# Kernel tuning notes

Hardware: AMD Instinct MI355X
Metric: run time of the kernel (lower is better)

The kernel has to match this reference:

```python
import jax, jax.numpy as jnp
import numpy as np

N = 50000        # nodes
E = 400000       # edges (no self-loops; self-loops appended in forward)
IN_DIM = 128
H, C = 4, 64     # heads, channels per head
D = H * C        # 256
NEG_SLOPE = 0.2


def setup_inputs() -> dict:
    key = jax.random.key(0)
    ks = jax.random.split(key, 8)
    x = jax.random.normal(ks[0], (N, IN_DIM), jnp.float32)
    # build edges with no self-loops (src != dst), matching the module's mask
    src = jax.random.randint(ks[1], (E,), 0, N)
    off = jax.random.randint(ks[2], (E,), 1, N)
    dst = (src + off) % N
    edge_index = jnp.stack([src, dst]).astype(jnp.int32)
    inp = {"x": x, "edge_index": edge_index}
    dims_in = [IN_DIM, D, D, D, D]
    for l in range(5):
        k = jax.random.split(ks[3 + l], 4)
        inp[f"W{l}"] = jax.random.normal(k[0], (D, dims_in[l]), jnp.float32) * 0.05
        inp[f"att_src{l}"] = jax.random.normal(k[1], (1, H, C), jnp.float32) * 0.05
        inp[f"att_dst{l}"] = jax.random.normal(k[2], (1, H, C), jnp.float32) * 0.05
        inp[f"bias{l}"] = jnp.zeros((D,), jnp.float32)
    return inp


def _gat_layer(x, W, a_src, a_dst, b, src, dst, relu_out):
    # linear projection, reshape to [N, H, C]
    h = (x @ W.T).reshape(N, H, C)
    alpha_src = jnp.sum(h * a_src, axis=-1)   # [N, H]
    alpha_dst = jnp.sum(h * a_dst, axis=-1)   # [N, H]
    # per-edge logits: alpha_j (source) + alpha_i (dest)
    alpha = jax.nn.leaky_relu(alpha_src[src] + alpha_dst[dst], negative_slope=NEG_SLOPE)  # [E', H]
    # segment softmax over destination neighborhoods (max is detached, as in the original)
    m = jax.lax.stop_gradient(jax.ops.segment_max(alpha, dst, num_segments=N))  # [N, H]
    e = jnp.exp(alpha - m[dst])
    s = jax.ops.segment_sum(e, dst, num_segments=N) + 1e-16
    a = e / s[dst]                                                             # [E', H]
    # weighted scatter-add aggregation of gathered source features
    out = jax.ops.segment_sum(a[:, :, None] * h[src], dst, num_segments=N)     # [N, H, C]
    out = out.reshape(N, D) + b
    return jax.nn.relu(out) if relu_out else out


def reference(x, edge_index,
              W0, att_src0, att_dst0, bias0,
              W1, att_src1, att_dst1, bias1,
              W2, att_src2, att_dst2, bias2,
              W3, att_src3, att_dst3, bias3,
              W4, att_src4, att_dst4, bias4):
    # input edges contain no self-loops; append one self-loop per node (as in the trace)
    loops = jnp.arange(N, dtype=edge_index.dtype)
    src = jnp.concatenate([edge_index[0], loops])
    dst = jnp.concatenate([edge_index[1], loops])
    params = [(W0, att_src0, att_dst0, bias0), (W1, att_src1, att_dst1, bias1),
              (W2, att_src2, att_dst2, bias2), (W3, att_src3, att_dst3, bias3),
              (W4, att_src4, att_dst4, bias4)]
    h = x
    for l, (W, a_s, a_d, b) in enumerate(params):
        h = _gat_layer(h, W, a_s, a_d, b, src, dst, relu_out=(l < 4))
    return h
```

## Files before the change

kernel.cpp:

```cpp
#include <hip/hip_runtime.h>
#include <hip/hip_bf16.h>

#define H 4
#define D 256
#define NEG_SLOPE 0.2f

typedef __attribute__((ext_vector_type(8))) _Float16 f16x8;
typedef __attribute__((ext_vector_type(4))) _Float16 f16x4;
typedef __attribute__((ext_vector_type(4))) float f32x4;

template<int K>
__device__ __forceinline__ void cvt_wfrag_one(const float* __restrict__ W,
                                              _Float16* __restrict__ wfrag, int idx) {
    const int NKS = K / 32;
    if (idx >= 16 * NKS * 64) return;
    int l  = idx & 63;
    int ks = (idx >> 6) % NKS;
    int c16 = idx / (NKS * 64);
    int col = c16 * 16 + (l & 15);
    int k0  = ks * 32 + (l >> 4) * 8;
    const float* src = &W[(size_t)col * K + k0];
    float4 v0 = *(const float4*)src;
    float4 v1 = *(const float4*)(src + 4);
    f16x8 o = {(_Float16)v0.x, (_Float16)v0.y, (_Float16)v0.z, (_Float16)v0.w,
               (_Float16)v1.x, (_Float16)v1.y, (_Float16)v1.z, (_Float16)v1.w};
    *(f16x8*)&wfrag[(size_t)idx * 8] = o;
}

__global__ void k_cvt_wfrag0(const float* __restrict__ W, _Float16* __restrict__ wfrag) {
    cvt_wfrag_one<128>(W, wfrag, blockIdx.x * blockDim.x + threadIdx.x);
}

__global__ void k_cvt_wfrag_all(const float* __restrict__ w1, const float* __restrict__ w2,
                                const float* __restrict__ w3, const float* __restrict__ w4,
                                _Float16* __restrict__ wfrag) {
    const float* ws[4] = {w1, w2, w3, w4};
    int l = blockIdx.y;
    cvt_wfrag_one<256>(ws[l], wfrag + 128 * 256 + (size_t)l * 256 * 256,
                       blockIdx.x * blockDim.x + threadIdx.x);
}

template<int K, bool F32X>
__global__ __launch_bounds__(256) void k_gemm_mfma(
        const void* __restrict__ xin, const _Float16* __restrict__ wfrag,
        const float* __restrict__ att_src, const float* __restrict__ att_dst,
        _Float16* __restrict__ hmat, float* __restrict__ alpha_src,
        float* __restrict__ alpha_dst, int nrows) {
    const int NKS = K / 32;
    __shared__ _Float16 sw[8 * NKS * 64 * 8];
    int t = threadIdx.x;
    int w = t >> 6, l = t & 63;
    int r = l & 15, q = l >> 4;
    int row0  = (blockIdx.x >> 1) * 64;
    int split = blockIdx.x & 1;

    {
        const uint4* wsrc = (const uint4*)(wfrag + (size_t)split * 8 * NKS * 64 * 8);
        uint4* wdst = (uint4*)sw;
        const int nchunk = 8 * NKS * 64;
        #pragma unroll
        for (int i = 0; i < nchunk / 256; ++i)
            wdst[i * 256 + t] = wsrc[i * 256 + t];
    }

    int gr_a = row0 + w * 16 + r;
    bool aok = (gr_a < nrows);
    f16x8 a[NKS];
    #pragma unroll
    for (int ks = 0; ks < NKS; ++ks) {
        if (aok) {
            if constexpr (F32X) {
                const float* xs = (const float*)xin + (size_t)gr_a * K + ks * 32 + q * 8;
                float4 v0 = *(const float4*)xs;
                float4 v1 = *(const float4*)(xs + 4);
                a[ks] = (f16x8){(_Float16)v0.x, (_Float16)v0.y, (_Float16)v0.z,
                                (_Float16)v0.w, (_Float16)v1.x, (_Float16)v1.y,
                                (_Float16)v1.z, (_Float16)v1.w};
            } else {
                a[ks] = *(const f16x8*)((const _Float16*)xin + (size_t)gr_a * K + ks * 32 + q * 8);
            }
        } else {
            a[ks] = (f16x8){0, 0, 0, 0, 0, 0, 0, 0};
        }
    }

    __syncthreads();

    f32x4 acc[8];
    #pragma unroll
    for (int cf = 0; cf < 8; ++cf) acc[cf] = (f32x4){0.f, 0.f, 0.f, 0.f};
    #pragma unroll
    for (int cf = 0; cf < 8; ++cf) {
        f16x8 b[NKS];
        #pragma unroll
        for (int ks = 0; ks < NKS; ++ks)
            b[ks] = *(f16x8*)&sw[(size_t)((cf * NKS + ks) * 64 + l) * 8];
        #pragma unroll
        for (int ks = 0; ks < NKS; ++ks)
            acc[cf] = __builtin_amdgcn_mfma_f32_16x16x32_f16(a[ks], b[ks], acc[cf], 0, 0, 0);
    }

    #pragma unroll
    for (int cf = 0; cf < 8; ++cf) {
        #pragma unroll
        for (int i = 0; i < 4; ++i) {
            int gr = row0 + w * 16 + q * 4 + i;
            if (gr < nrows)
                hmat[(size_t)gr * D + split * 128 + cf * 16 + r] = (_Float16)acc[cf][i];
        }
    }
    float asv[8], adv[8];
    #pragma unroll
    for (int cf = 0; cf < 8; ++cf) {
        asv[cf] = att_src[split * 128 + cf * 16 + r];
        adv[cf] = att_dst[split * 128 + cf * 16 + r];
    }
    #pragma unroll
    for (int i = 0; i < 4; ++i) {
        #pragma unroll
        for (int hh = 0; hh < 2; ++hh) {
            float ps = 0.f, pd = 0.f;
            #pragma unroll
            for (int j = 0; j < 4; ++j) {
                int cf = hh * 4 + j;
                ps += acc[cf][i] * asv[cf];
                pd += acc[cf][i] * adv[cf];
            }
            #pragma unroll
            for (int m = 1; m < 16; m <<= 1) {
                ps += __shfl_xor(ps, m);
                pd += __shfl_xor(pd, m);
            }
            int gr = row0 + w * 16 + q * 4 + i;
            if (r == 0 && gr < nrows) {
                alpha_src[gr * 4 + split * 2 + hh] = ps;
                alpha_dst[gr * 4 + split * 2 + hh] = pd;
            }
        }
    }
}

__global__ void k_deg(const int* __restrict__ ei, int E, int E2, int* __restrict__ deg) {
    int e = blockIdx.x * blockDim.x + threadIdx.x;
    if (e >= E2) return;
    int de = (e < E) ? ei[E + e] : (e - E);
    atomicAdd(&deg[de], 1);
}

__global__ void k_scan_block(const int* __restrict__ deg, int* __restrict__ incl,
                             int* __restrict__ bsum, int n) {
    __shared__ int sd[256];
    int t = threadIdx.x;
    int i = blockIdx.x * 256 + t;
    int v = (i < n) ? deg[i] : 0;
    sd[t] = v;
    __syncthreads();
    for (int off = 1; off < 256; off <<= 1) {
        int add = (t >= off) ? sd[t - off] : 0;
        __syncthreads();
        sd[t] += add;
        __syncthreads();
    }
    if (i < n) incl[i] = sd[t];
    if (t == 255) bsum[blockIdx.x] = sd[255];
}

__global__ void k_scan_bsum(int* __restrict__ bsum, int nb) {
    __shared__ int sd[256];
    int t = threadIdx.x;
    int v = (t < nb) ? bsum[t] : 0;
    sd[t] = v;
    __syncthreads();
    for (int off = 1; off < 256; off <<= 1) {
        int add = (t >= off) ? sd[t - off] : 0;
        __syncthreads();
        sd[t] += add;
        __syncthreads();
    }
    if (t < nb) bsum[t] = sd[t] - v;
}

__global__ void k_rowptr(const int* __restrict__ incl, const int* __restrict__ deg,
                         const int* __restrict__ boff, int* __restrict__ row_ptr,
                         int n, int total) {
    int i = blockIdx.x * blockDim.x + threadIdx.x;
    if (i < n) row_ptr[i] = incl[i] - deg[i] + boff[i >> 8];
    if (i == 0) row_ptr[n] = total;
}

__global__ void k_scatter(const int* __restrict__ ei, int E, int E2,
                          const int* __restrict__ row_ptr, int* __restrict__ cursor,
                          int* __restrict__ csr_src) {
    int e = blockIdx.x * blockDim.x + threadIdx.x;
    if (e >= E2) return;
    int se, de;
    if (e < E) { se = ei[e]; de = ei[E + e]; }
    else       { se = e - E; de = se; }
    int pos = atomicAdd(&cursor[de], 1);
    csr_src[row_ptr[de] + pos] = se;
}

__global__ __launch_bounds__(256) void k_aggregate(const _Float16* __restrict__ hmat,
        const int* __restrict__ row_ptr, const int* __restrict__ csr_src,
        const float* __restrict__ alpha_src, const float* __restrict__ alpha_dst,
        const float* __restrict__ bias, float* __restrict__ outf,
        _Float16* __restrict__ outx, int relu, int nrows) {
    int wid  = (blockIdx.x * 256 + threadIdx.x) >> 6;
    int lane = threadIdx.x & 63;
    int node = wid * 2 + (lane >> 5);
    if (node >= nrows) return;
    int c    = lane & 31;
    int head = c >> 3;
    int st = row_ptr[node], en = row_ptr[node + 1];
    int deg = en - st;
    int nbatch = (deg + 7) >> 3;
    float a_d = alpha_dst[node * 4 + head];
    float acc[8] = {};
    float ssum = 0.f;
    int sn[8];
    #pragma unroll
    for (int j = 0; j < 8; ++j) {
        int li = st + (j < deg ? j : deg - 1);
        sn[j] = csr_src[li];
    }
    for (int b = 0; b < nbatch; ++b) {
        f16x8 hv[8];
        #pragma unroll
        for (int j = 0; j < 8; ++j)
            hv[j] = *(const f16x8*)&hmat[(size_t)sn[j] * D + c * 8];
        float as[8];
        #pragma unroll
        for (int j = 0; j < 8; ++j) as[j] = alpha_src[sn[j] * 4 + head];
        int sn2[8];
        if (b + 1 < nbatch) {
            #pragma unroll
            for (int j = 0; j < 8; ++j) {
                int e = (b + 1) * 8 + j;
                int li = st + (e < deg ? e : deg - 1);
                sn2[j] = csr_src[li];
            }
        }
        #pragma unroll
        for (int j = 0; j < 8; ++j) {
            float a = as[j] + a_d;
            a = a > 0.f ? a : NEG_SLOPE * a;
            float ex = (b * 8 + j < deg) ? __expf(a) : 0.f;
            ssum += ex;
            #pragma unroll
            for (int k = 0; k < 8; ++k) acc[k] += ex * (float)hv[j][k];
        }
        #pragma unroll
        for (int j = 0; j < 8; ++j) sn[j] = sn2[j];
    }
    float sinv = 1.f / (ssum + 1e-16f);
    float4 b0 = *(const float4*)&bias[c * 8];
    float4 b1 = *(const float4*)&bias[c * 8 + 4];
    float o[8];
    o[0] = acc[0] * sinv + b0.x; o[1] = acc[1] * sinv + b0.y;
    o[2] = acc[2] * sinv + b0.z; o[3] = acc[3] * sinv + b0.w;
    o[4] = acc[4] * sinv + b1.x; o[5] = acc[5] * sinv + b1.y;
    o[6] = acc[6] * sinv + b1.z; o[7] = acc[7] * sinv + b1.w;
    if (relu) {
        #pragma unroll
        for (int k = 0; k < 8; ++k) o[k] = fmaxf(o[k], 0.f);
    }
    if (outx) {
        f16x8 o8 = {(_Float16)o[0], (_Float16)o[1], (_Float16)o[2], (_Float16)o[3],
                    (_Float16)o[4], (_Float16)o[5], (_Float16)o[6], (_Float16)o[7]};
        *(f16x8*)&outx[(size_t)node * D + c * 8] = o8;
    } else {
        *(float4*)&outf[(size_t)node * D + c * 8] =
            make_float4(o[0], o[1], o[2], o[3]);
        *(float4*)&outf[(size_t)node * D + c * 8 + 4] =
            make_float4(o[4], o[5], o[6], o[7]);
    }
}

extern "C" void kernel_launch(void* const* d_in, const int* in_sizes, int n_in,
                              void* d_out, int out_size, void* d_ws, size_t ws_size,
                              hipStream_t stream) {
    const float* x = (const float*)d_in[0];
    const int* ei = (const int*)d_in[1];
    const int N  = in_sizes[0] / 128;
    const int E  = in_sizes[1] / 2;
    const int E2 = E + N;

    char* wsp = (char*)d_ws;
    size_t off = 0;
    auto alloc = [&](size_t bytes) -> void* {
        void* p = wsp + off;
        off += (bytes + 255) & ~(size_t)255;
        return p;
    };
    _Float16* bufH  = (_Float16*)alloc((size_t)N * D * 2);
    _Float16* xf16  = (_Float16*)alloc((size_t)N * D * 2);
    _Float16* wfrag = (_Float16*)alloc((size_t)(128 * 256 + 4 * 256 * 256) * 2);
    float* alpha_src = (float*)alloc((size_t)N * H * 4);
    float* alpha_dst = (float*)alloc((size_t)N * H * 4);
    int*   deg       = (int*)alloc((size_t)N * 4);
    int*   incl      = (int*)alloc((size_t)N * 4);
    int*   bsum      = (int*)alloc(256 * 4);
    int*   row_ptr   = (int*)alloc((size_t)(N + 1) * 4);
    int*   cursor    = (int*)alloc((size_t)N * 4);
    int*   csr_src   = (int*)alloc((size_t)E2 * 4);
    (void)ws_size;

    hipMemsetAsync(deg, 0, (size_t)N * 4, stream);
    hipMemsetAsync(cursor, 0, (size_t)N * 4, stream);

    k_cvt_wfrag0<<<(16 * 4 * 64 + 255) / 256, 256, 0, stream>>>(
        (const float*)d_in[2], wfrag);
    dim3 wg((16 * 8 * 64 + 255) / 256, 4);
    k_cvt_wfrag_all<<<wg, 256, 0, stream>>>(
        (const float*)d_in[6], (const float*)d_in[10],
        (const float*)d_in[14], (const float*)d_in[18], wfrag);

    int egrid = (E2 + 255) / 256;
    k_deg<<<egrid, 256, 0, stream>>>(ei, E, E2, deg);
    int nb = (N + 255) / 256;
    k_scan_block<<<nb, 256, 0, stream>>>(deg, incl, bsum, N);
    k_scan_bsum<<<1, 256, 0, stream>>>(bsum, nb);
    k_rowptr<<<nb, 256, 0, stream>>>(incl, deg, bsum, row_ptr, N, E2);
    k_scatter<<<egrid, 256, 0, stream>>>(ei, E, E2, row_ptr, cursor, csr_src);

    int ggrid = ((N + 63) / 64) * 2;
    int agrid = (N + 7) / 8;
    for (int l = 0; l < 5; ++l) {
        const float* as_ = (const float*)d_in[3 + 4 * l];
        const float* ad_ = (const float*)d_in[4 + 4 * l];
        const float* bs_ = (const float*)d_in[5 + 4 * l];
        const _Float16* wl = (l == 0) ? wfrag
                           : wfrag + 128 * 256 + (size_t)(l - 1) * 256 * 256;

        if (l == 0)
            k_gemm_mfma<128, true><<<ggrid, 256, 0, stream>>>(x, wl, as_, ad_,
                                                        bufH, alpha_src, alpha_dst, N);
        else
            k_gemm_mfma<256, false><<<ggrid, 256, 0, stream>>>(xf16, wl, as_, ad_,
                                                        bufH, alpha_src, alpha_dst, N);

        int last = (l == 4);
        k_aggregate<<<agrid, 256, 0, stream>>>(bufH, row_ptr, csr_src,
                                               alpha_src, alpha_dst, bs_,
                                               last ? (float*)d_out : nullptr,
                                               last ? nullptr : xf16,
                                               last ? 0 : 1, N);
    }
}
```

Measured before the change: 392.3 us.

## Split GEMM output into four head-sized column blocks with XCD-aware block mapping

The projection GEMM now gives each workgroup one head (64 columns) instead of half the output, which doubles the grid and halves the shared-memory weight tile and accumulator registers. Block IDs are remapped so that groups of eight consecutive blocks cover eight different row chunks, likely to spread the A-row reuse across the chiplets. The cursor memset is folded into the rowptr kernel to save one launch. In exchange, each A row is loaded four times instead of twice, adding input reads.

```diff
diff --git a/kernel.cpp b/kernel.cpp
--- a/kernel.cpp
+++ b/kernel.cpp
@@ -45,21 +45,33 @@
         const void* __restrict__ xin, const _Float16* __restrict__ wfrag,
         const float* __restrict__ att_src, const float* __restrict__ att_dst,
         _Float16* __restrict__ hmat, float* __restrict__ alpha_src,
-        float* __restrict__ alpha_dst, int nrows) {
+        float* __restrict__ alpha_dst, int nrows, int nchunk) {
     const int NKS = K / 32;
-    __shared__ _Float16 sw[8 * NKS * 64 * 8];
+    __shared__ _Float16 sw[4 * NKS * 64 * 8];
     int t = threadIdx.x;
     int w = t >> 6, l = t & 63;
     int r = l & 15, q = l >> 4;
-    int row0  = (blockIdx.x >> 1) * 64;
-    int split = blockIdx.x & 1;
+
+    int bid = blockIdx.x;
+    int nfull = (nchunk >> 3) << 3;
+    int dmain = nfull * 4;
+    int chunk, split;
+    if (bid < dmain) {
+        int j = bid >> 3;
+        chunk = (bid & 7) + 8 * (j >> 2);
+        split = j & 3;
+    } else {
+        int idx = bid - dmain;
+        chunk = nfull + (idx >> 2);
+        split = idx & 3;
+    }
+    int row0 = chunk * 64;
 
     {
-        const uint4* wsrc = (const uint4*)(wfrag + (size_t)split * 8 * NKS * 64 * 8);
+        const uint4* wsrc = (const uint4*)(wfrag + (size_t)split * 4 * NKS * 64 * 8);
         uint4* wdst = (uint4*)sw;
-        const int nchunk = 8 * NKS * 64;
-        #pragma unroll
-        for (int i = 0; i < nchunk / 256; ++i)
+        #pragma unroll
+        for (int i = 0; i < NKS; ++i)
             wdst[i * 256 + t] = wsrc[i * 256 + t];
     }
 
@@ -86,11 +98,11 @@
 
     __syncthreads();
 
-    f32x4 acc[8];
-    #pragma unroll
-    for (int cf = 0; cf < 8; ++cf) acc[cf] = (f32x4){0.f, 0.f, 0.f, 0.f};
-    #pragma unroll
-    for (int cf = 0; cf < 8; ++cf) {
+    f32x4 acc[4];
+    #pragma unroll
+    for (int cf = 0; cf < 4; ++cf) acc[cf] = (f32x4){0.f, 0.f, 0.f, 0.f};
+    #pragma unroll
+    for (int cf = 0; cf < 4; ++cf) {
         f16x8 b[NKS];
         #pragma unroll
         for (int ks = 0; ks < NKS; ++ks)
@@ -101,41 +113,37 @@
     }
 
     #pragma unroll
-    for (int cf = 0; cf < 8; ++cf) {
+    for (int cf = 0; cf < 4; ++cf) {
         #pragma unroll
         for (int i = 0; i < 4; ++i) {
             int gr = row0 + w * 16 + q * 4 + i;
             if (gr < nrows)
-                hmat[(size_t)gr * D + split * 128 + cf * 16 + r] = (_Float16)acc[cf][i];
-        }
-    }
-    float asv[8], adv[8];
-    #pragma unroll
-    for (int cf = 0; cf < 8; ++cf) {
-        asv[cf] = att_src[split * 128 + cf * 16 + r];
-        adv[cf] = att_dst[split * 128 + cf * 16 + r];
+                hmat[(size_t)gr * D + split * 64 + cf * 16 + r] = (_Float16)acc[cf][i];
+        }
+    }
+    float asv[4], adv[4];
+    #pragma unroll
+    for (int cf = 0; cf < 4; ++cf) {
+        asv[cf] = att_src[split * 64 + cf * 16 + r];
+        adv[cf] = att_dst[split * 64 + cf * 16 + r];
     }
     #pragma unroll
     for (int i = 0; i < 4; ++i) {
-        #pragma unroll
-        for (int hh = 0; hh < 2; ++hh) {
-            float ps = 0.f, pd = 0.f;
-            #pragma unroll
-            for (int j = 0; j < 4; ++j) {
-                int cf = hh * 4 + j;
-                ps += acc[cf][i] * asv[cf];
-                pd += acc[cf][i] * adv[cf];
-            }
-            #pragma unroll
-            for (int m = 1; m < 16; m <<= 1) {
-                ps += __shfl_xor(ps, m);
-                pd += __shfl_xor(pd, m);
-            }
-            int gr = row0 + w * 16 + q * 4 + i;
-            if (r == 0 && gr < nrows) {
-                alpha_src[gr * 4 + split * 2 + hh] = ps;
-                alpha_dst[gr * 4 + split * 2 + hh] = pd;
-            }
+        float ps = 0.f, pd = 0.f;
+        #pragma unroll
+        for (int cf = 0; cf < 4; ++cf) {
+            ps += acc[cf][i] * asv[cf];
+            pd += acc[cf][i] * adv[cf];
+        }
+        #pragma unroll
+        for (int m = 1; m < 16; m <<= 1) {
+            ps += __shfl_xor(ps, m);
+            pd += __shfl_xor(pd, m);
+        }
+        int gr = row0 + w * 16 + q * 4 + i;
+        if (r == 0 && gr < nrows) {
+            alpha_src[gr * 4 + split] = ps;
+            alpha_dst[gr * 4 + split] = pd;
         }
     }
 }
@@ -182,9 +190,12 @@
 
 __global__ void k_rowptr(const int* __restrict__ incl, const int* __restrict__ deg,
                          const int* __restrict__ boff, int* __restrict__ row_ptr,
-                         int n, int total) {
+                         int* __restrict__ cursor, int n, int total) {
     int i = blockIdx.x * blockDim.x + threadIdx.x;
-    if (i < n) row_ptr[i] = incl[i] - deg[i] + boff[i >> 8];
+    if (i < n) {
+        row_ptr[i] = incl[i] - deg[i] + boff[i >> 8];
+        cursor[i] = 0;
+    }
     if (i == 0) row_ptr[n] = total;
 }
 
@@ -306,7 +317,6 @@
     (void)ws_size;
 
     hipMemsetAsync(deg, 0, (size_t)N * 4, stream);
-    hipMemsetAsync(cursor, 0, (size_t)N * 4, stream);
 
     k_cvt_wfrag0<<<(16 * 4 * 64 + 255) / 256, 256, 0, stream>>>(
         (const float*)d_in[2], wfrag);
@@ -320,10 +330,11 @@
     int nb = (N + 255) / 256;
     k_scan_block<<<nb, 256, 0, stream>>>(deg, incl, bsum, N);
     k_scan_bsum<<<1, 256, 0, stream>>>(bsum, nb);
-    k_rowptr<<<nb, 256, 0, stream>>>(incl, deg, bsum, row_ptr, N, E2);
+    k_rowptr<<<nb, 256, 0, stream>>>(incl, deg, bsum, row_ptr, cursor, N, E2);
     k_scatter<<<egrid, 256, 0, stream>>>(ei, E, E2, row_ptr, cursor, csr_src);
 
-    int ggrid = ((N + 63) / 64) * 2;
+    int nchunk = (N + 63) / 64;
+    int ggrid = nchunk * 4;
     int agrid = (N + 7) / 8;
     for (int l = 0; l < 5; ++l) {
         const float* as_ = (const float*)d_in[3 + 4 * l];
@@ -334,10 +345,10 @@
 
         if (l == 0)
             k_gemm_mfma<128, true><<<ggrid, 256, 0, stream>>>(x, wl, as_, ad_,
-                                                        bufH, alpha_src, alpha_dst, N);
+                                                        bufH, alpha_src, alpha_dst, N, nchunk);
         else
             k_gemm_mfma<256, false><<<ggrid, 256, 0, stream>>>(xf16, wl, as_, ad_,
-                                                        bufH, alpha_src, alpha_dst, N);
+                                                        bufH, alpha_src, alpha_dst, N, nchunk);
 
         int last = (l == 4);
         k_aggregate<<<agrid, 256, 0, stream>>>(bufH, row_ptr, csr_src,
```

Result: faster. 374.5 us, median of 2 (-4.5%).
